# Kernel tuning notes

Hardware: AMD Instinct MI355X
Metric: run time of the kernel (lower is better)

## Reference

```python
import jax, jax.numpy as jnp
import numpy as np
import math

N_ANGLES = 8
HIGH_FREQ_RATIO = 0.3


def setup_inputs() -> dict:
    key = jax.random.key(0)
    k1, k2 = jax.random.split(key)
    x = jax.random.normal(k1, (4, 256, 256, 256), dtype=jnp.float32)
    # learnable per-angle weights, init near enhance_init=1.0 with small perturbation
    angle_weights = 1.0 + 0.1 * jax.random.normal(k2, (N_ANGLES,), dtype=jnp.float32)
    return {"x": x, "angle_weights": angle_weights}


def _angle_gain(H, W, angle_weights):
    # Build [H, W] real gain: angle-sector weight in the high-frequency band, 1 elsewhere.
    cy, cx = H // 2, W // 2
    y = jnp.arange(H, dtype=jnp.float32)[:, None] - cy
    x = jnp.arange(W, dtype=jnp.float32)[None, :] - cx
    r = jnp.sqrt(y * y + x * x)
    theta = jnp.arctan2(y, x) + math.pi  # [0, 2*pi]
    angle_step = 2.0 * math.pi / N_ANGLES
    angle_idx = jnp.mod(jnp.floor(theta / angle_step).astype(jnp.int32), N_ANGLES)
    r_max = min(cy, cx)
    high_freq_mask = r > HIGH_FREQ_RATIO * r_max
    weights = angle_weights[angle_idx]  # [H, W]
    return jnp.where(high_freq_mask, weights, jnp.ones_like(weights))


def reference(x, angle_weights):
    # x: [B, C, H, W]
    H, W = x.shape[-2], x.shape[-1]
    gain = _angle_gain(H, W, angle_weights)  # [H, W], real
    xf = jnp.fft.fftshift(jnp.fft.fft2(x, norm="ortho"), axes=(-2, -1))
    # mag*gain * exp(i*phase) == gain * (mag*exp(i*phase)) == gain * spectrum (gain real)
    xf_enh = xf * gain
    x_enh = jnp.fft.ifft2(jnp.fft.ifftshift(xf_enh, axes=(-2, -1)), norm="ortho").real
    return x + x_enh
```

## Files before the change

### kernel.cpp

```cpp
#include <hip/hip_runtime.h>
#include <math.h>

#define PI_F 3.14159265358979323846f

__device__ __forceinline__ float2 cmul(float2 a, float2 b) {
    return make_float2(a.x * b.x - a.y * b.y, a.x * b.y + a.y * b.x);
}
__device__ __forceinline__ float2 cmulc(float2 a, float2 b) {
    return make_float2(a.x * b.x + a.y * b.y, a.y * b.x - a.x * b.y);
}
__device__ __forceinline__ int digitrev4(int p) {
    return ((p & 3) << 6) | (((p >> 2) & 3) << 4) | (((p >> 4) & 3) << 2) | ((p >> 6) & 3);
}

template<int S>
__device__ __forceinline__ void stage_fwd(float2* line, int stride, int j, const float2* lut) {
    const int h = 1 << (2 * S);
    int k  = j & (h - 1);
    int B  = j >> (2 * S);
    int i0 = (B << (2 * S + 2)) + k;
    float2 a0 = line[(i0        ) * stride];
    float2 a1 = line[(i0 +     h) * stride];
    float2 a2 = line[(i0 + 2 * h) * stride];
    float2 a3 = line[(i0 + 3 * h) * stride];
    float2 t0 = make_float2(a0.x + a2.x, a0.y + a2.y);
    float2 t1 = make_float2(a0.x - a2.x, a0.y - a2.y);
    float2 t2 = make_float2(a1.x + a3.x, a1.y + a3.y);
    float2 u  = make_float2(a1.x - a3.x, a1.y - a3.y);
    float2 t3 = make_float2(u.y, -u.x);
    int eu = k << (6 - 2 * S);
    line[(i0        ) * stride] = make_float2(t0.x + t2.x, t0.y + t2.y);
    line[(i0 +     h) * stride] = cmul(make_float2(t1.x + t3.x, t1.y + t3.y), lut[eu]);
    line[(i0 + 2 * h) * stride] = cmul(make_float2(t0.x - t2.x, t0.y - t2.y), lut[2 * eu]);
    line[(i0 + 3 * h) * stride] = cmul(make_float2(t1.x - t3.x, t1.y - t3.y), lut[3 * eu]);
}

template<int S>
__device__ __forceinline__ void stage_inv(float2* line, int stride, int j, const float2* lut) {
    const int h = 1 << (2 * S);
    int k  = j & (h - 1);
    int B  = j >> (2 * S);
    int i0 = (B << (2 * S + 2)) + k;
    int eu = k << (6 - 2 * S);
    float2 b0 = line[(i0        ) * stride];
    float2 b1 = cmulc(line[(i0 +     h) * stride], lut[eu]);
    float2 b2 = cmulc(line[(i0 + 2 * h) * stride], lut[2 * eu]);
    float2 b3 = cmulc(line[(i0 + 3 * h) * stride], lut[3 * eu]);
    float2 t0 = make_float2(b0.x + b2.x, b0.y + b2.y);
    float2 t1 = make_float2(b0.x - b2.x, b0.y - b2.y);
    float2 t2 = make_float2(b1.x + b3.x, b1.y + b3.y);
    float2 u  = make_float2(b1.x - b3.x, b1.y - b3.y);
    float2 t3 = make_float2(-u.y, u.x);
    line[(i0        ) * stride] = make_float2(t0.x + t2.x, t0.y + t2.y);
    line[(i0 +     h) * stride] = make_float2(t1.x + t3.x, t1.y + t3.y);
    line[(i0 + 2 * h) * stride] = make_float2(t0.x - t2.x, t0.y - t2.y);
    line[(i0 + 3 * h) * stride] = make_float2(t1.x - t3.x, t1.y - t3.y);
}

__device__ __forceinline__ void build_lut(float2* lut, int t) {
    float ang = -2.0f * PI_F * (float)t * (1.0f / 256.0f);
    float sn, cs;
    __sincosf(ang, &sn, &cs);
    lut[t] = make_float2(cs, sn);
}

__device__ __forceinline__ float gain1(float fy, float fx, const float* sw) {
    float r2 = fy * fy + fx * fx;
    float theta = atan2f(fy, fx) + PI_F;
    int idx = ((int)floorf(theta * (4.0f / PI_F))) & 7;
    float wv = sw[idx];
    return (r2 > 1474.56f) ? wv : 1.0f;
}

__global__ __launch_bounds__(256) void k_fft_rows(const float* __restrict__ x, float* __restrict__ out) {
    __shared__ float2 lut[256];
    __shared__ float2 lds[4][256];
    int t = threadIdx.x;
    build_lut(lut, t);
    __syncthreads();
    int q    = blockIdx.x >> 6;
    int rg   = blockIdx.x & 63;
    int wv   = t >> 6, lane = t & 63;
    int h    = rg * 4 + wv;
    int plane = ((q >> 7) * 256) + ((q & 127) * 2);
    size_t rowA = ((size_t)plane << 16) + ((size_t)h << 8);
    size_t rowB = rowA + 65536;
    float2* line = lds[wv];
    {
        int w = lane * 4;
        float4 re = *(const float4*)(x + rowA + w);
        float4 im = *(const float4*)(x + rowB + w);
        line[w + 0] = make_float2(re.x, im.x);
        line[w + 1] = make_float2(re.y, im.y);
        line[w + 2] = make_float2(re.z, im.z);
        line[w + 3] = make_float2(re.w, im.w);
    }
    __syncthreads();
    stage_fwd<3>(line, 1, lane, lut); __syncthreads();
    stage_fwd<2>(line, 1, lane, lut); __syncthreads();
    stage_fwd<1>(line, 1, lane, lut); __syncthreads();
    stage_fwd<0>(line, 1, lane, lut); __syncthreads();
    {
        int w = lane * 4;
        float4 re = make_float4(line[w].x, line[w + 1].x, line[w + 2].x, line[w + 3].x);
        float4 im = make_float4(line[w].y, line[w + 1].y, line[w + 2].y, line[w + 3].y);
        *(float4*)(out + rowA + w) = re;
        *(float4*)(out + rowB + w) = im;
    }
}

__global__ __launch_bounds__(256) void k_fft_cols(float* __restrict__ data, const float* __restrict__ wts) {
    __shared__ float2 lut[256];
    __shared__ float2 tile[256][17];
    __shared__ float  sw[8];
    int t = threadIdx.x;
    build_lut(lut, t);
    if (t < 8) sw[t] = wts[t];
    __syncthreads();
    int q  = blockIdx.x >> 4;
    int wt = blockIdx.x & 15;
    int w0 = wt * 16;
    int plane = ((q >> 7) * 256) + ((q & 127) * 2);
    size_t baseA = ((size_t)plane << 16) + (size_t)w0;
    size_t baseB = baseA + 65536;
#pragma unroll
    for (int it = 0; it < 4; ++it) {
        int hh = it * 64 + (t >> 2);
        int cc = (t & 3) * 4;
        float4 re = *(const float4*)(data + baseA + hh * 256 + cc);
        float4 im = *(const float4*)(data + baseB + hh * 256 + cc);
        tile[hh][cc + 0] = make_float2(re.x, im.x);
        tile[hh][cc + 1] = make_float2(re.y, im.y);
        tile[hh][cc + 2] = make_float2(re.z, im.z);
        tile[hh][cc + 3] = make_float2(re.w, im.w);
    }
    __syncthreads();
    int c = t & 15, g = t >> 4;
    float2* line = &tile[0][c];
    { for (int i2 = 0; i2 < 4; ++i2) stage_fwd<3>(line, 17, g * 4 + i2, lut); } __syncthreads();
    { for (int i2 = 0; i2 < 4; ++i2) stage_fwd<2>(line, 17, g * 4 + i2, lut); } __syncthreads();
    { for (int i2 = 0; i2 < 4; ++i2) stage_fwd<1>(line, 17, g * 4 + i2, lut); } __syncthreads();
    { for (int i2 = 0; i2 < 4; ++i2) stage_fwd<0>(line, 17, g * 4 + i2, lut); } __syncthreads();
    {
        int kw = digitrev4(w0 + c);
        float fx  = (kw < 128) ? (float)kw : (float)(kw - 256);
        float fx2 = (kw == 128) ? -128.0f : -fx;
#pragma unroll
        for (int it = 0; it < 16; ++it) {
            int hh = it * 16 + g;
            int kh = digitrev4(hh);
            float fy  = (kh < 128) ? (float)kh : (float)(kh - 256);
            float fy2 = (kh == 128) ? -128.0f : -fy;
            float g1 = gain1(fy, fx, sw);
            float g2 = gain1(fy2, fx2, sw);
            float sc = (1.0f + 0.5f * (g1 + g2)) * (1.0f / 65536.0f);
            float2 v = line[hh * 17];
            line[hh * 17] = make_float2(v.x * sc, v.y * sc);
        }
    }
    __syncthreads();
    { for (int i2 = 0; i2 < 4; ++i2) stage_inv<0>(line, 17, g * 4 + i2, lut); } __syncthreads();
    { for (int i2 = 0; i2 < 4; ++i2) stage_inv<1>(line, 17, g * 4 + i2, lut); } __syncthreads();
    { for (int i2 = 0; i2 < 4; ++i2) stage_inv<2>(line, 17, g * 4 + i2, lut); } __syncthreads();
    { for (int i2 = 0; i2 < 4; ++i2) stage_inv<3>(line, 17, g * 4 + i2, lut); } __syncthreads();
#pragma unroll
    for (int it = 0; it < 4; ++it) {
        int hh = it * 64 + (t >> 2);
        int cc = (t & 3) * 4;
        float4 re = make_float4(tile[hh][cc].x, tile[hh][cc + 1].x, tile[hh][cc + 2].x, tile[hh][cc + 3].x);
        float4 im = make_float4(tile[hh][cc].y, tile[hh][cc + 1].y, tile[hh][cc + 2].y, tile[hh][cc + 3].y);
        *(float4*)(data + baseA + hh * 256 + cc) = re;
        *(float4*)(data + baseB + hh * 256 + cc) = im;
    }
}

__global__ __launch_bounds__(256) void k_ifft_rows(float* __restrict__ data) {
    __shared__ float2 lut[256];
    __shared__ float2 lds[4][256];
    int t = threadIdx.x;
    build_lut(lut, t);
    __syncthreads();
    int q    = blockIdx.x >> 6;
    int rg   = blockIdx.x & 63;
    int wv   = t >> 6, lane = t & 63;
    int h    = rg * 4 + wv;
    int plane = ((q >> 7) * 256) + ((q & 127) * 2);
    size_t rowA = ((size_t)plane << 16) + ((size_t)h << 8);
    size_t rowB = rowA + 65536;
    float2* line = lds[wv];
    {
        int w = lane * 4;
        float4 re = *(const float4*)(data + rowA + w);
        float4 im = *(const float4*)(data + rowB + w);
        line[w + 0] = make_float2(re.x, im.x);
        line[w + 1] = make_float2(re.y, im.y);
        line[w + 2] = make_float2(re.z, im.z);
        line[w + 3] = make_float2(re.w, im.w);
    }
    __syncthreads();
    stage_inv<0>(line, 1, lane, lut); __syncthreads();
    stage_inv<1>(line, 1, lane, lut); __syncthreads();
    stage_inv<2>(line, 1, lane, lut); __syncthreads();
    stage_inv<3>(line, 1, lane, lut); __syncthreads();
    {
        int w = lane * 4;
        float4 re = make_float4(line[w].x, line[w + 1].x, line[w + 2].x, line[w + 3].x);
        float4 im = make_float4(line[w].y, line[w + 1].y, line[w + 2].y, line[w + 3].y);
        *(float4*)(data + rowA + w) = re;
        *(float4*)(data + rowB + w) = im;
    }
}

extern "C" void kernel_launch(void* const* d_in, const int* in_sizes, int n_in,
                              void* d_out, int out_size, void* d_ws, size_t ws_size,
                              hipStream_t stream) {
    const float* x   = (const float*)d_in[0];
    const float* wts = (const float*)d_in[1];
    float* out = (float*)d_out;
    (void)in_sizes; (void)n_in; (void)d_ws; (void)ws_size; (void)out_size;
    k_fft_rows <<<512 * 64, 256, 0, stream>>>(x, out);
    k_fft_cols <<<512 * 16, 256, 0, stream>>>(out, wts);
    k_ifft_rows<<<512 * 64, 256, 0, stream>>>(out);
}
```

Before: 662.8 us.

## Restructure FFT kernels: per-wave lines, register twiddles, gain LUT, transposed column tile

Replaces block-wide barriers with wave-local LDS waits by giving each wavefront its own lines: two rows per wave in the row passes, and a full column per group of lanes in the column pass. Twiddles are computed in registers with sincos instead of a shared LUT. The column tile is transposed so each column is contiguous, with vectorized float4 LDS accesses. The spectral gain is precomputed once into a workspace table. The code relies on wave-synchronous execution being correct, and the new twiddle math and layouts add extra ALU work and possible bank conflicts.

```diff
diff --git a/kernel.cpp b/kernel.cpp
--- a/kernel.cpp
+++ b/kernel.cpp
@@ -2,6 +2,7 @@
 #include <math.h>
 
 #define PI_F 3.14159265358979323846f
+#define WSYNC() asm volatile("s_waitcnt lgkmcnt(0)" ::: "memory")
 
 __device__ __forceinline__ float2 cmul(float2 a, float2 b) {
     return make_float2(a.x * b.x - a.y * b.y, a.x * b.y + a.y * b.x);
@@ -12,56 +13,48 @@
 __device__ __forceinline__ int digitrev4(int p) {
     return ((p & 3) << 6) | (((p >> 2) & 3) << 4) | (((p >> 4) & 3) << 2) | ((p >> 6) & 3);
 }
-
-template<int S>
-__device__ __forceinline__ void stage_fwd(float2* line, int stride, int j, const float2* lut) {
+__device__ __forceinline__ void tw3(int eu, float2& w1, float2& w2, float2& w3) {
+    float sn, cs;
+    __sincosf(-(2.0f * PI_F / 256.0f) * (float)eu, &sn, &cs);
+    w1 = make_float2(cs, sn);
+    w2 = cmul(w1, w1);
+    w3 = cmul(w2, w1);
+}
+
+template<int S>
+__device__ __forceinline__ void stage_fwd_j(float2* line, int j, float2 w1, float2 w2, float2 w3) {
     const int h = 1 << (2 * S);
     int k  = j & (h - 1);
-    int B  = j >> (2 * S);
-    int i0 = (B << (2 * S + 2)) + k;
-    float2 a0 = line[(i0        ) * stride];
-    float2 a1 = line[(i0 +     h) * stride];
-    float2 a2 = line[(i0 + 2 * h) * stride];
-    float2 a3 = line[(i0 + 3 * h) * stride];
+    int i0 = ((j >> (2 * S)) << (2 * S + 2)) + k;
+    float2 a0 = line[i0], a1 = line[i0 + h], a2 = line[i0 + 2 * h], a3 = line[i0 + 3 * h];
     float2 t0 = make_float2(a0.x + a2.x, a0.y + a2.y);
     float2 t1 = make_float2(a0.x - a2.x, a0.y - a2.y);
     float2 t2 = make_float2(a1.x + a3.x, a1.y + a3.y);
     float2 u  = make_float2(a1.x - a3.x, a1.y - a3.y);
     float2 t3 = make_float2(u.y, -u.x);
-    int eu = k << (6 - 2 * S);
-    line[(i0        ) * stride] = make_float2(t0.x + t2.x, t0.y + t2.y);
-    line[(i0 +     h) * stride] = cmul(make_float2(t1.x + t3.x, t1.y + t3.y), lut[eu]);
-    line[(i0 + 2 * h) * stride] = cmul(make_float2(t0.x - t2.x, t0.y - t2.y), lut[2 * eu]);
-    line[(i0 + 3 * h) * stride] = cmul(make_float2(t1.x - t3.x, t1.y - t3.y), lut[3 * eu]);
-}
-
-template<int S>
-__device__ __forceinline__ void stage_inv(float2* line, int stride, int j, const float2* lut) {
+    line[i0]         = make_float2(t0.x + t2.x, t0.y + t2.y);
+    line[i0 + h]     = cmul(make_float2(t1.x + t3.x, t1.y + t3.y), w1);
+    line[i0 + 2 * h] = cmul(make_float2(t0.x - t2.x, t0.y - t2.y), w2);
+    line[i0 + 3 * h] = cmul(make_float2(t1.x - t3.x, t1.y - t3.y), w3);
+}
+template<int S>
+__device__ __forceinline__ void stage_inv_j(float2* line, int j, float2 w1, float2 w2, float2 w3) {
     const int h = 1 << (2 * S);
     int k  = j & (h - 1);
-    int B  = j >> (2 * S);
-    int i0 = (B << (2 * S + 2)) + k;
-    int eu = k << (6 - 2 * S);
-    float2 b0 = line[(i0        ) * stride];
-    float2 b1 = cmulc(line[(i0 +     h) * stride], lut[eu]);
-    float2 b2 = cmulc(line[(i0 + 2 * h) * stride], lut[2 * eu]);
-    float2 b3 = cmulc(line[(i0 + 3 * h) * stride], lut[3 * eu]);
+    int i0 = ((j >> (2 * S)) << (2 * S + 2)) + k;
+    float2 b0 = line[i0];
+    float2 b1 = cmulc(line[i0 + h], w1);
+    float2 b2 = cmulc(line[i0 + 2 * h], w2);
+    float2 b3 = cmulc(line[i0 + 3 * h], w3);
     float2 t0 = make_float2(b0.x + b2.x, b0.y + b2.y);
     float2 t1 = make_float2(b0.x - b2.x, b0.y - b2.y);
     float2 t2 = make_float2(b1.x + b3.x, b1.y + b3.y);
     float2 u  = make_float2(b1.x - b3.x, b1.y - b3.y);
     float2 t3 = make_float2(-u.y, u.x);
-    line[(i0        ) * stride] = make_float2(t0.x + t2.x, t0.y + t2.y);
-    line[(i0 +     h) * stride] = make_float2(t1.x + t3.x, t1.y + t3.y);
-    line[(i0 + 2 * h) * stride] = make_float2(t0.x - t2.x, t0.y - t2.y);
-    line[(i0 + 3 * h) * stride] = make_float2(t1.x - t3.x, t1.y - t3.y);
-}
-
-__device__ __forceinline__ void build_lut(float2* lut, int t) {
-    float ang = -2.0f * PI_F * (float)t * (1.0f / 256.0f);
-    float sn, cs;
-    __sincosf(ang, &sn, &cs);
-    lut[t] = make_float2(cs, sn);
+    line[i0]         = make_float2(t0.x + t2.x, t0.y + t2.y);
+    line[i0 + h]     = make_float2(t1.x + t3.x, t1.y + t3.y);
+    line[i0 + 2 * h] = make_float2(t0.x - t2.x, t0.y - t2.y);
+    line[i0 + 3 * h] = make_float2(t1.x - t3.x, t1.y - t3.y);
 }
 
 __device__ __forceinline__ float gain1(float fy, float fx, const float* sw) {
@@ -72,143 +65,211 @@
     return (r2 > 1474.56f) ? wv : 1.0f;
 }
 
-__global__ __launch_bounds__(256) void k_fft_rows(const float* __restrict__ x, float* __restrict__ out) {
-    __shared__ float2 lut[256];
-    __shared__ float2 lds[4][256];
+__global__ __launch_bounds__(256) void k_gain_lut(const float* __restrict__ wts, float* __restrict__ lut2) {
+    __shared__ float sw[8];
+    int h = threadIdx.x, w = blockIdx.x;
+    if (h < 8) sw[h] = wts[h];
+    __syncthreads();
+    int kw = digitrev4(w), kh = digitrev4(h);
+    float fx  = (kw < 128) ? (float)kw : (float)(kw - 256);
+    float fx2 = (kw == 128) ? -128.0f : -fx;
+    float fy  = (kh < 128) ? (float)kh : (float)(kh - 256);
+    float fy2 = (kh == 128) ? -128.0f : -fy;
+    float g1 = gain1(fy, fx, sw);
+    float g2 = gain1(fy2, fx2, sw);
+    lut2[w * 256 + h] = (1.0f + 0.5f * (g1 + g2)) * (1.0f / 65536.0f);
+}
+
+__global__ __launch_bounds__(256) void k_row_fwd(const float* __restrict__ x, float* __restrict__ out) {
+    __shared__ float2 lds[8][256];
+    int t = threadIdx.x, wv = t >> 6, lane = t & 63;
+    int gr = blockIdx.x * 8 + wv * 2;
+    int q = gr >> 8, h = gr & 255;
+    int plane = ((q >> 7) << 8) + ((q & 127) << 1);
+    size_t rA = ((size_t)plane << 16) + ((size_t)h << 8);
+    size_t rB = rA + 65536;
+    float2* L0 = lds[wv * 2];
+    float2* L1 = lds[wv * 2 + 1];
+    int w = lane * 4;
+    float4 re0 = *(const float4*)(x + rA + w);
+    float4 im0 = *(const float4*)(x + rB + w);
+    float4 re1 = *(const float4*)(x + rA + 256 + w);
+    float4 im1 = *(const float4*)(x + rB + 256 + w);
+    *(float4*)&L0[w]     = make_float4(re0.x, im0.x, re0.y, im0.y);
+    *(float4*)&L0[w + 2] = make_float4(re0.z, im0.z, re0.w, im0.w);
+    *(float4*)&L1[w]     = make_float4(re1.x, im1.x, re1.y, im1.y);
+    *(float4*)&L1[w + 2] = make_float4(re1.z, im1.z, re1.w, im1.w);
+    WSYNC();
+    { float2 w1,w2,w3; tw3((lane & 63) << 0, w1,w2,w3);
+      stage_fwd_j<3>(L0, lane, w1,w2,w3); stage_fwd_j<3>(L1, lane, w1,w2,w3); WSYNC(); }
+    { float2 w1,w2,w3; tw3((lane & 15) << 2, w1,w2,w3);
+      stage_fwd_j<2>(L0, lane, w1,w2,w3); stage_fwd_j<2>(L1, lane, w1,w2,w3); WSYNC(); }
+    { float2 w1,w2,w3; tw3((lane & 3) << 4, w1,w2,w3);
+      stage_fwd_j<1>(L0, lane, w1,w2,w3); stage_fwd_j<1>(L1, lane, w1,w2,w3); WSYNC(); }
+    { float2 one = make_float2(1.0f, 0.0f);
+      stage_fwd_j<0>(L0, lane, one,one,one); stage_fwd_j<0>(L1, lane, one,one,one); WSYNC(); }
+    float4 a0 = *(float4*)&L0[w], a1 = *(float4*)&L0[w + 2];
+    float4 b0 = *(float4*)&L1[w], b1 = *(float4*)&L1[w + 2];
+    *(float4*)(out + rA + w)       = make_float4(a0.x, a0.z, a1.x, a1.z);
+    *(float4*)(out + rB + w)       = make_float4(a0.y, a0.w, a1.y, a1.w);
+    *(float4*)(out + rA + 256 + w) = make_float4(b0.x, b0.z, b1.x, b1.z);
+    *(float4*)(out + rB + 256 + w) = make_float4(b0.y, b0.w, b1.y, b1.w);
+}
+
+template<int S>
+__device__ __forceinline__ void col_stage_fwd(float2* line, int jb) {
+#pragma unroll
+    for (int i2 = 0; i2 < 4; ++i2) {
+        int j = jb + 16 * i2;
+        int k = j & ((1 << (2 * S)) - 1);
+        float2 w1,w2,w3; tw3(k << (6 - 2 * S), w1,w2,w3);
+        stage_fwd_j<S>(line, j, w1,w2,w3);
+    }
+}
+template<int S>
+__device__ __forceinline__ void col_stage_inv(float2* line, int jb) {
+#pragma unroll
+    for (int i2 = 0; i2 < 4; ++i2) {
+        int j = jb + 16 * i2;
+        int k = j & ((1 << (2 * S)) - 1);
+        float2 w1,w2,w3; tw3(k << (6 - 2 * S), w1,w2,w3);
+        stage_inv_j<S>(line, j, w1,w2,w3);
+    }
+}
+
+template<bool USE_LUT>
+__global__ __launch_bounds__(256) void k_col(float* __restrict__ data,
+                                            const float* __restrict__ lut2,
+                                            const float* __restrict__ wts) {
+    __shared__ float2 tile[16][258];
+    __shared__ float sw[8];
     int t = threadIdx.x;
-    build_lut(lut, t);
-    __syncthreads();
-    int q    = blockIdx.x >> 6;
-    int rg   = blockIdx.x & 63;
-    int wv   = t >> 6, lane = t & 63;
-    int h    = rg * 4 + wv;
-    int plane = ((q >> 7) * 256) + ((q & 127) * 2);
-    size_t rowA = ((size_t)plane << 16) + ((size_t)h << 8);
-    size_t rowB = rowA + 65536;
-    float2* line = lds[wv];
-    {
-        int w = lane * 4;
-        float4 re = *(const float4*)(x + rowA + w);
-        float4 im = *(const float4*)(x + rowB + w);
-        line[w + 0] = make_float2(re.x, im.x);
-        line[w + 1] = make_float2(re.y, im.y);
-        line[w + 2] = make_float2(re.z, im.z);
-        line[w + 3] = make_float2(re.w, im.w);
-    }
-    __syncthreads();
-    stage_fwd<3>(line, 1, lane, lut); __syncthreads();
-    stage_fwd<2>(line, 1, lane, lut); __syncthreads();
-    stage_fwd<1>(line, 1, lane, lut); __syncthreads();
-    stage_fwd<0>(line, 1, lane, lut); __syncthreads();
-    {
-        int w = lane * 4;
-        float4 re = make_float4(line[w].x, line[w + 1].x, line[w + 2].x, line[w + 3].x);
-        float4 im = make_float4(line[w].y, line[w + 1].y, line[w + 2].y, line[w + 3].y);
-        *(float4*)(out + rowA + w) = re;
-        *(float4*)(out + rowB + w) = im;
-    }
-}
-
-__global__ __launch_bounds__(256) void k_fft_cols(float* __restrict__ data, const float* __restrict__ wts) {
-    __shared__ float2 lut[256];
-    __shared__ float2 tile[256][17];
-    __shared__ float  sw[8];
-    int t = threadIdx.x;
-    build_lut(lut, t);
-    if (t < 8) sw[t] = wts[t];
-    __syncthreads();
-    int q  = blockIdx.x >> 4;
-    int wt = blockIdx.x & 15;
-    int w0 = wt * 16;
-    int plane = ((q >> 7) * 256) + ((q & 127) * 2);
+    if (!USE_LUT && t < 8) sw[t] = wts[t];
+    int q = blockIdx.x >> 4, wt = blockIdx.x & 15, w0 = wt * 16;
+    int plane = ((q >> 7) << 8) + ((q & 127) << 1);
     size_t baseA = ((size_t)plane << 16) + (size_t)w0;
     size_t baseB = baseA + 65536;
-#pragma unroll
-    for (int it = 0; it < 4; ++it) {
-        int hh = it * 64 + (t >> 2);
-        int cc = (t & 3) * 4;
-        float4 re = *(const float4*)(data + baseA + hh * 256 + cc);
-        float4 im = *(const float4*)(data + baseB + hh * 256 + cc);
-        tile[hh][cc + 0] = make_float2(re.x, im.x);
-        tile[hh][cc + 1] = make_float2(re.y, im.y);
-        tile[hh][cc + 2] = make_float2(re.z, im.z);
-        tile[hh][cc + 3] = make_float2(re.w, im.w);
+    int c0 = (t & 3) * 4, h0 = (t >> 2) * 4;
+    {
+        float4 reR[4], imR[4];
+#pragma unroll
+        for (int r = 0; r < 4; ++r) {
+            reR[r] = *(const float4*)(data + baseA + (size_t)(h0 + r) * 256 + c0);
+            imR[r] = *(const float4*)(data + baseB + (size_t)(h0 + r) * 256 + c0);
+        }
+#pragma unroll
+        for (int k = 0; k < 4; ++k) {
+            float r0 = (&reR[0].x)[k], i0v = (&imR[0].x)[k];
+            float r1 = (&reR[1].x)[k], i1v = (&imR[1].x)[k];
+            float r2 = (&reR[2].x)[k], i2v = (&imR[2].x)[k];
+            float r3 = (&reR[3].x)[k], i3v = (&imR[3].x)[k];
+            *(float4*)&tile[c0 + k][h0]     = make_float4(r0, i0v, r1, i1v);
+            *(float4*)&tile[c0 + k][h0 + 2] = make_float4(r2, i2v, r3, i3v);
+        }
     }
     __syncthreads();
-    int c = t & 15, g = t >> 4;
-    float2* line = &tile[0][c];
-    { for (int i2 = 0; i2 < 4; ++i2) stage_fwd<3>(line, 17, g * 4 + i2, lut); } __syncthreads();
-    { for (int i2 = 0; i2 < 4; ++i2) stage_fwd<2>(line, 17, g * 4 + i2, lut); } __syncthreads();
-    { for (int i2 = 0; i2 < 4; ++i2) stage_fwd<1>(line, 17, g * 4 + i2, lut); } __syncthreads();
-    { for (int i2 = 0; i2 < 4; ++i2) stage_fwd<0>(line, 17, g * 4 + i2, lut); } __syncthreads();
+    int wv = t >> 6, lane = t & 63;
+    int col = wv * 4 + (lane & 3);
+    int jb  = lane >> 2;
+    float2* line = tile[col];
+    col_stage_fwd<3>(line, jb); WSYNC();
+    col_stage_fwd<2>(line, jb); WSYNC();
+    col_stage_fwd<1>(line, jb); WSYNC();
+    col_stage_fwd<0>(line, jb); WSYNC();
     {
-        int kw = digitrev4(w0 + c);
-        float fx  = (kw < 128) ? (float)kw : (float)(kw - 256);
-        float fx2 = (kw == 128) ? -128.0f : -fx;
-#pragma unroll
-        for (int it = 0; it < 16; ++it) {
-            int hh = it * 16 + g;
-            int kh = digitrev4(hh);
-            float fy  = (kh < 128) ? (float)kh : (float)(kh - 256);
-            float fy2 = (kh == 128) ? -128.0f : -fy;
-            float g1 = gain1(fy, fx, sw);
-            float g2 = gain1(fy2, fx2, sw);
-            float sc = (1.0f + 0.5f * (g1 + g2)) * (1.0f / 65536.0f);
-            float2 v = line[hh * 17];
-            line[hh * 17] = make_float2(v.x * sc, v.y * sc);
-        }
-    }
+        int hb = jb * 16;
+        if (USE_LUT) {
+            const float* lp = lut2 + (size_t)(w0 + col) * 256 + hb;
+#pragma unroll
+            for (int ch = 0; ch < 4; ++ch) {
+                float4 s4 = *(const float4*)(lp + ch * 4);
+#pragma unroll
+                for (int e = 0; e < 4; ++e) {
+                    int hh = hb + ch * 4 + e;
+                    float sc = (&s4.x)[e];
+                    float2 v = line[hh];
+                    line[hh] = make_float2(v.x * sc, v.y * sc);
+                }
+            }
+        } else {
+            int kw = digitrev4(w0 + col);
+            float fx  = (kw < 128) ? (float)kw : (float)(kw - 256);
+            float fx2 = (kw == 128) ? -128.0f : -fx;
+#pragma unroll
+            for (int m = 0; m < 16; ++m) {
+                int hh = hb + m;
+                int kh = digitrev4(hh);
+                float fy  = (kh < 128) ? (float)kh : (float)(kh - 256);
+                float fy2 = (kh == 128) ? -128.0f : -fy;
+                float g1 = gain1(fy, fx, sw);
+                float g2 = gain1(fy2, fx2, sw);
+                float sc = (1.0f + 0.5f * (g1 + g2)) * (1.0f / 65536.0f);
+                float2 v = line[hh];
+                line[hh] = make_float2(v.x * sc, v.y * sc);
+            }
+        }
+        WSYNC();
+    }
+    col_stage_inv<0>(line, jb); WSYNC();
+    col_stage_inv<1>(line, jb); WSYNC();
+    col_stage_inv<2>(line, jb); WSYNC();
+    col_stage_inv<3>(line, jb); WSYNC();
     __syncthreads();
-    { for (int i2 = 0; i2 < 4; ++i2) stage_inv<0>(line, 17, g * 4 + i2, lut); } __syncthreads();
-    { for (int i2 = 0; i2 < 4; ++i2) stage_inv<1>(line, 17, g * 4 + i2, lut); } __syncthreads();
-    { for (int i2 = 0; i2 < 4; ++i2) stage_inv<2>(line, 17, g * 4 + i2, lut); } __syncthreads();
-    { for (int i2 = 0; i2 < 4; ++i2) stage_inv<3>(line, 17, g * 4 + i2, lut); } __syncthreads();
-#pragma unroll
-    for (int it = 0; it < 4; ++it) {
-        int hh = it * 64 + (t >> 2);
-        int cc = (t & 3) * 4;
-        float4 re = make_float4(tile[hh][cc].x, tile[hh][cc + 1].x, tile[hh][cc + 2].x, tile[hh][cc + 3].x);
-        float4 im = make_float4(tile[hh][cc].y, tile[hh][cc + 1].y, tile[hh][cc + 2].y, tile[hh][cc + 3].y);
-        *(float4*)(data + baseA + hh * 256 + cc) = re;
-        *(float4*)(data + baseB + hh * 256 + cc) = im;
-    }
-}
-
-__global__ __launch_bounds__(256) void k_ifft_rows(float* __restrict__ data) {
-    __shared__ float2 lut[256];
-    __shared__ float2 lds[4][256];
-    int t = threadIdx.x;
-    build_lut(lut, t);
-    __syncthreads();
-    int q    = blockIdx.x >> 6;
-    int rg   = blockIdx.x & 63;
-    int wv   = t >> 6, lane = t & 63;
-    int h    = rg * 4 + wv;
-    int plane = ((q >> 7) * 256) + ((q & 127) * 2);
-    size_t rowA = ((size_t)plane << 16) + ((size_t)h << 8);
-    size_t rowB = rowA + 65536;
-    float2* line = lds[wv];
     {
-        int w = lane * 4;
-        float4 re = *(const float4*)(data + rowA + w);
-        float4 im = *(const float4*)(data + rowB + w);
-        line[w + 0] = make_float2(re.x, im.x);
-        line[w + 1] = make_float2(re.y, im.y);
-        line[w + 2] = make_float2(re.z, im.z);
-        line[w + 3] = make_float2(re.w, im.w);
-    }
-    __syncthreads();
-    stage_inv<0>(line, 1, lane, lut); __syncthreads();
-    stage_inv<1>(line, 1, lane, lut); __syncthreads();
-    stage_inv<2>(line, 1, lane, lut); __syncthreads();
-    stage_inv<3>(line, 1, lane, lut); __syncthreads();
-    {
-        int w = lane * 4;
-        float4 re = make_float4(line[w].x, line[w + 1].x, line[w + 2].x, line[w + 3].x);
-        float4 im = make_float4(line[w].y, line[w + 1].y, line[w + 2].y, line[w + 3].y);
-        *(float4*)(data + rowA + w) = re;
-        *(float4*)(data + rowB + w) = im;
-    }
+        float2 v[4][4];
+#pragma unroll
+        for (int k = 0; k < 4; ++k) {
+            float4 lo = *(float4*)&tile[c0 + k][h0];
+            float4 hi = *(float4*)&tile[c0 + k][h0 + 2];
+            v[k][0] = make_float2(lo.x, lo.y);
+            v[k][1] = make_float2(lo.z, lo.w);
+            v[k][2] = make_float2(hi.x, hi.y);
+            v[k][3] = make_float2(hi.z, hi.w);
+        }
+#pragma unroll
+        for (int r = 0; r < 4; ++r) {
+            *(float4*)(data + baseA + (size_t)(h0 + r) * 256 + c0) =
+                make_float4(v[0][r].x, v[1][r].x, v[2][r].x, v[3][r].x);
+            *(float4*)(data + baseB + (size_t)(h0 + r) * 256 + c0) =
+                make_float4(v[0][r].y, v[1][r].y, v[2][r].y, v[3][r].y);
+        }
+    }
+}
+
+__global__ __launch_bounds__(256) void k_row_inv(float* __restrict__ data) {
+    __shared__ float2 lds[8][256];
+    int t = threadIdx.x, wv = t >> 6, lane = t & 63;
+    int gr = blockIdx.x * 8 + wv * 2;
+    int q = gr >> 8, h = gr & 255;
+    int plane = ((q >> 7) << 8) + ((q & 127) << 1);
+    size_t rA = ((size_t)plane << 16) + ((size_t)h << 8);
+    size_t rB = rA + 65536;
+    float2* L0 = lds[wv * 2];
+    float2* L1 = lds[wv * 2 + 1];
+    int w = lane * 4;
+    float4 re0 = *(const float4*)(data + rA + w);
+    float4 im0 = *(const float4*)(data + rB + w);
+    float4 re1 = *(const float4*)(data + rA + 256 + w);
+    float4 im1 = *(const float4*)(data + rB + 256 + w);
+    *(float4*)&L0[w]     = make_float4(re0.x, im0.x, re0.y, im0.y);
+    *(float4*)&L0[w + 2] = make_float4(re0.z, im0.z, re0.w, im0.w);
+    *(float4*)&L1[w]     = make_float4(re1.x, im1.x, re1.y, im1.y);
+    *(float4*)&L1[w + 2] = make_float4(re1.z, im1.z, re1.w, im1.w);
+    WSYNC();
+    { float2 one = make_float2(1.0f, 0.0f);
+      stage_inv_j<0>(L0, lane, one,one,one); stage_inv_j<0>(L1, lane, one,one,one); WSYNC(); }
+    { float2 w1,w2,w3; tw3((lane & 3) << 4, w1,w2,w3);
+      stage_inv_j<1>(L0, lane, w1,w2,w3); stage_inv_j<1>(L1, lane, w1,w2,w3); WSYNC(); }
+    { float2 w1,w2,w3; tw3((lane & 15) << 2, w1,w2,w3);
+      stage_inv_j<2>(L0, lane, w1,w2,w3); stage_inv_j<2>(L1, lane, w1,w2,w3); WSYNC(); }
+    { float2 w1,w2,w3; tw3((lane & 63) << 0, w1,w2,w3);
+      stage_inv_j<3>(L0, lane, w1,w2,w3); stage_inv_j<3>(L1, lane, w1,w2,w3); WSYNC(); }
+    float4 a0 = *(float4*)&L0[w], a1 = *(float4*)&L0[w + 2];
+    float4 b0 = *(float4*)&L1[w], b1 = *(float4*)&L1[w + 2];
+    *(float4*)(data + rA + w)       = make_float4(a0.x, a0.z, a1.x, a1.z);
+    *(float4*)(data + rB + w)       = make_float4(a0.y, a0.w, a1.y, a1.w);
+    *(float4*)(data + rA + 256 + w) = make_float4(b0.x, b0.z, b1.x, b1.z);
+    *(float4*)(data + rB + 256 + w) = make_float4(b0.y, b0.w, b1.y, b1.w);
 }
 
 extern "C" void kernel_launch(void* const* d_in, const int* in_sizes, int n_in,
@@ -217,8 +278,16 @@
     const float* x   = (const float*)d_in[0];
     const float* wts = (const float*)d_in[1];
     float* out = (float*)d_out;
-    (void)in_sizes; (void)n_in; (void)d_ws; (void)ws_size; (void)out_size;
-    k_fft_rows <<<512 * 64, 256, 0, stream>>>(x, out);
-    k_fft_cols <<<512 * 16, 256, 0, stream>>>(out, wts);
-    k_ifft_rows<<<512 * 64, 256, 0, stream>>>(out);
-}
+    (void)in_sizes; (void)n_in; (void)out_size;
+    bool use_lut = (ws_size >= 256 * 256 * sizeof(float)) && (d_ws != nullptr);
+    if (use_lut) {
+        k_gain_lut<<<256, 256, 0, stream>>>(wts, (float*)d_ws);
+    }
+    k_row_fwd<<<16384, 256, 0, stream>>>(x, out);
+    if (use_lut) {
+        k_col<true><<<8192, 256, 0, stream>>>(out, (const float*)d_ws, wts);
+    } else {
+        k_col<false><<<8192, 256, 0, stream>>>(out, nullptr, wts);
+    }
+    k_row_inv<<<16384, 256, 0, stream>>>(out);
+}
```

Measured after the change: 658.3 us. Within noise of the previous version (-0.7%).
